# Optimization experiments

Measured on AMD Instinct MI355X. Metric: run time of the kernel, lower is better.

The kernel has to match this reference:

```python
import jax, jax.numpy as jnp
import numpy as np

B, S, I, H, HI = 1024, 64, 2048, 2048, 2048  # batch, num_high_states, input_dim, hidden_dim, high_dim
L = 4          # num recurrent layers
NH = 16        # num heads
HD = H // NH   # head dim
MAX_STEPS = 100


def setup_inputs() -> dict:
    key = jax.random.key(0)
    ks = iter(jax.random.split(key, 40))
    std = 0.02
    d = {}
    d["x"] = jax.random.normal(next(ks), (B, I), jnp.float32)
    d["high_state"] = jax.random.normal(next(ks), (B, HI), jnp.float32)
    d["high_states_history"] = jax.random.normal(next(ks), (B, S, HI), jnp.float32)
    d["hidden"] = jax.random.normal(next(ks), (L, B, H), jnp.float32) * 0.1
    # input projection + timestep embedding
    d["W_in"] = jax.random.normal(next(ks), (I, H), jnp.float32) * std
    d["b_in"] = jnp.zeros((H,), jnp.float32)
    d["ts_emb"] = jax.random.normal(next(ks), (MAX_STEPS, H), jnp.float32) * std
    # hierarchical attention projections
    d["Wq"] = jax.random.normal(next(ks), (H, H), jnp.float32) * std
    d["bq"] = jnp.zeros((H,), jnp.float32)
    d["Wk"] = jax.random.normal(next(ks), (HI, H), jnp.float32) * std
    d["bk"] = jnp.zeros((H,), jnp.float32)
    d["Wv"] = jax.random.normal(next(ks), (HI, H), jnp.float32) * std
    d["bv"] = jnp.zeros((H,), jnp.float32)
    d["Wo"] = jax.random.normal(next(ks), (H, H), jnp.float32) * std
    d["bo"] = jnp.zeros((H,), jnp.float32)
    # per-layer GRU-like gates, stacked over layers; Linear in = I+H = 2H
    for nm in ("Wu", "Wr", "Ws", "Wc"):
        d[nm] = jax.random.normal(next(ks), (L, 2 * H, H), jnp.float32) * std
    for nm in ("bu", "br", "bs", "bc"):
        d[nm] = jnp.zeros((L, H), jnp.float32)
    # layer norm
    d["ln_g"] = jnp.ones((H,), jnp.float32)
    d["ln_b"] = jnp.zeros((H,), jnp.float32)
    d["timestep"] = 5
    return d


def _forward(x, high_states_history, hidden, W_in, b_in, ts_emb,
             Wq, bq, Wk, bk, Wv, bv, Wo, bo,
             Wu, bu, Wr, br, Ws, bs, Wc, bc, ln_g, ln_b, timestep):
    # input projection + timestep encoding
    x = x @ W_in + b_in + ts_emb[timestep]  # [B,H]
    # hierarchical attention (single query per batch element)
    q = (x @ Wq + bq).reshape(B, NH, HD)
    k = (high_states_history @ Wk + bk).reshape(B, S, NH, HD)
    v = (high_states_history @ Wv + bv).reshape(B, S, NH, HD)
    scores = jnp.einsum("bhd,bshd->bhs", q, k) / np.sqrt(HD).astype(np.float32)
    attn = jax.nn.softmax(scores, axis=-1)  # [B,NH,S]
    ctx = jnp.einsum("bhs,bshd->bhd", attn, v).reshape(B, H)
    x = x + (ctx @ Wo + bo)
    # stacked GRU-like recurrent layers (loop over fixed small L)
    new_hidden = []
    for i in range(L):
        h = hidden[i]
        comb = jnp.concatenate([x, h], axis=1)  # [B,2H]
        u = jax.nn.sigmoid(comb @ Wu[i] + bu[i])
        r = jax.nn.sigmoid(comb @ Wr[i] + br[i])
        s = jax.nn.sigmoid(comb @ Ws[i] + bs[i])
        comb_r = jnp.concatenate([x, r * h], axis=1)
        cand = jax.nn.gelu(comb_r @ Wc[i] + bc[i], approximate=False)
        new_h = (1 - u) * h + u * (s * cand + (1 - s) * h)
        new_hidden.append(new_h)
        x = new_h  # dropout is identity in eval
    # layer norm (eps matches torch default 1e-5)
    mu = jnp.mean(x, axis=-1, keepdims=True)
    var = jnp.mean(jnp.square(x - mu), axis=-1, keepdims=True)
    out = (x - mu) * jax.lax.rsqrt(var + 1e-5) * ln_g + ln_b
    return out, jnp.stack(new_hidden)


def reference(x, high_state, high_states_history, hidden, W_in, b_in, ts_emb,
              Wq, bq, Wk, bk, Wv, bv, Wo, bo,
              Wu, bu, Wr, br, Ws, bs, Wc, bc, ln_g, ln_b, timestep):
    # high_state is accepted by the original signature but unused in the body
    return _forward(x, high_states_history, hidden, W_in, b_in, ts_emb,
                    Wq, bq, Wk, bk, Wv, bv, Wo, bo,
                    Wu, bu, Wr, br, Ws, bs, Wc, bc, ln_g, ln_b, timestep)
```

## Files before the change

kernel.cpp:

```cpp
#include <hip/hip_runtime.h>
#include <hip/hip_bf16.h>
#include <math.h>

#define B_  1024
#define S_  64
#define H_  2048
#define L_  4
#define NH_ 16
#define HD_ 128
#define WSLAB_ ((size_t)2048 * 4096)

typedef __attribute__((ext_vector_type(4))) float floatx4;
typedef __attribute__((ext_vector_type(8))) short shortx8;

__device__ __forceinline__ unsigned short f2bf(float f) {
  union { float f; unsigned int u; } v; v.f = f;
  unsigned int u = v.u;
  return (unsigned short)((u + 0x7fffu + ((u >> 16) & 1u)) >> 16);
}

__device__ __forceinline__ void gload16(const void* g, void* l) {
  __builtin_amdgcn_global_load_lds(
      (const __attribute__((address_space(1))) void*)g,
      (__attribute__((address_space(3))) void*)l, 16, 0, 0);
}

__global__ __launch_bounds__(256) void cvt_bf(
    const float* __restrict__ in, unsigned short* __restrict__ out, int n8)
{
  int i = blockIdx.x * 256 + threadIdx.x;
  if (i >= n8) return;
  const float4* p = (const float4*)in;
  float4 a = p[i * 2], b = p[i * 2 + 1];
  unsigned short o[8] = { f2bf(a.x), f2bf(a.y), f2bf(a.z), f2bf(a.w),
                          f2bf(b.x), f2bf(b.y), f2bf(b.z), f2bf(b.w) };
  ((uint4*)out)[i] = *(uint4*)o;
}

__global__ __launch_bounds__(256) void tconv4(
    const float* __restrict__ s0, const float* __restrict__ s1,
    const float* __restrict__ s2, const float* __restrict__ s3,
    unsigned short* __restrict__ dst, int K)
{
  const float* src = (blockIdx.z == 0) ? s0 : (blockIdx.z == 1) ? s1
                   : (blockIdx.z == 2) ? s2 : s3;
  unsigned short* out = dst + (size_t)blockIdx.z * 2048 * K;
  __shared__ float tile[64][65];
  int k0 = blockIdx.x * 64, n0 = blockIdx.y * 64;
  int t = threadIdx.x;
  int tr = t >> 4, tc = (t & 15) * 4;
  #pragma unroll
  for (int rep = 0; rep < 4; ++rep) {
    int kk = tr + rep * 16;
    float4 v = *(const float4*)(src + (size_t)(k0 + kk) * 2048 + n0 + tc);
    tile[kk][tc] = v.x; tile[kk][tc + 1] = v.y;
    tile[kk][tc + 2] = v.z; tile[kk][tc + 3] = v.w;
  }
  __syncthreads();
  int nr = t >> 2, kc = (t & 3) * 16;
  unsigned short o[16];
  #pragma unroll
  for (int j = 0; j < 16; ++j) o[j] = f2bf(tile[kc + j][nr]);
  *(uint4*)(out + (size_t)(n0 + nr) * K + k0 + kc)     = *(uint4*)&o[0];
  *(uint4*)(out + (size_t)(n0 + nr) * K + k0 + kc + 8) = *(uint4*)&o[8];
}

enum { EPI_XIN = 0, EPI_QB = 1, EPI_X2 = 2, EPI_GRU = 3, EPI_CTX = 4 };

template<int EPI>
__global__ __launch_bounds__(512) void gemm_w(
    int K, int bpitch, int koff,
    const unsigned short* __restrict__ A0,
    const unsigned short* __restrict__ BT,
    const float* __restrict__ b0,
    const float* __restrict__ tse, const int* __restrict__ tsp,
    const float* __restrict__ res,
    const float* __restrict__ Cc, const float* __restrict__ U,
    const float* __restrict__ Sg, const float* __restrict__ Hf,
    float* __restrict__ Cf, unsigned short* __restrict__ Cb)
{
  const int t = threadIdx.x, wid = t >> 6, lane = t & 63, lr = lane & 15, lg = lane >> 4;
  const int wr = wid >> 2, wc = wid & 3;
  const int g = blockIdx.x;
  const int m_base = (g >> 4) * 64;
  const int pn = g & 15;
  __shared__ unsigned short lds_a[64 * 32];
  __shared__ unsigned short lds_b[128 * 32];
  floatx4 acc[2][2] = {};
  const int arow = t >> 2, akc = t & 3;
  const int akcs = akc ^ ((arow >> 1) & 3);
  const int brow = t >> 2, bkc = t & 3;
  const int bkcs = bkc ^ ((brow >> 1) & 3);
  const int nkt = K >> 5;
  for (int kt = 0; kt < nkt; ++kt) {
    if (t < 256) {
      int gk = kt * 32 + akcs * 8;
      const unsigned short* ga;
      if (EPI == EPI_CTX) ga = A0 + ((size_t)(m_base + arow) * 16 + pn) * 2048 + gk;
      else                ga = A0 + (size_t)(m_base + arow) * K + gk;
      gload16(ga, &lds_a[wid * 512]);
    }
    {
      int gk = kt * 32 + bkcs * 8;
      const unsigned short* gb;
      if (EPI == EPI_CTX) gb = BT + (size_t)(pn * 128 + brow) * 2048 + gk;
      else                gb = BT + (size_t)((pn & 15) * 128 + brow) * bpitch + koff + gk;
      gload16(gb, &lds_b[wid * 512]);
    }
    __syncthreads();
    const int sl = lg ^ ((lr >> 1) & 3);
    shortx8 af[2], bfv[2];
    #pragma unroll
    for (int mt = 0; mt < 2; ++mt)
      af[mt] = *(shortx8*)&lds_a[(wr * 32 + mt * 16 + lr) * 32 + sl * 8];
    #pragma unroll
    for (int nt = 0; nt < 2; ++nt)
      bfv[nt] = *(shortx8*)&lds_b[(wc * 32 + nt * 16 + lr) * 32 + sl * 8];
    #pragma unroll
    for (int mt = 0; mt < 2; ++mt)
      #pragma unroll
      for (int nt = 0; nt < 2; ++nt)
        acc[mt][nt] = __builtin_amdgcn_mfma_f32_16x16x32_bf16(af[mt], bfv[nt], acc[mt][nt], 0, 0, 0);
    __syncthreads();
  }
  int ts = 0;
  if (EPI == EPI_XIN) ts = tsp[0];
  #pragma unroll
  for (int mt = 0; mt < 2; ++mt)
  #pragma unroll
  for (int nt = 0; nt < 2; ++nt)
  #pragma unroll
  for (int j = 0; j < 4; ++j) {
    int row = m_base + wr * 32 + mt * 16 + lg * 4 + j;
    int col = pn * 128 + wc * 32 + nt * 16 + lr;
    size_t idx = (size_t)row * 2048 + col;
    float v = acc[mt][nt][j] + b0[col];
    if (EPI == EPI_XIN) {
      v += tse[(size_t)ts * 2048 + col];
      Cf[idx] = v; Cb[idx] = f2bf(v);
    } else if (EPI == EPI_QB) {
      Cb[idx] = f2bf(v);
    } else if (EPI == EPI_X2) {
      v += res[idx]; Cb[idx] = f2bf(v);
    } else if (EPI == EPI_CTX) {
      Cb[idx] = f2bf(v);
    } else {
      v += Cc[idx];
      float gl = 0.5f * v * (1.f + erff(v * 0.70710678118654752f));
      float u = U[idx], s = Sg[idx], hh = Hf[idx];
      float nh = (1.f - u) * hh + u * (s * gl + (1.f - s) * hh);
      Cf[idx] = nh; Cb[idx] = f2bf(nh);
    }
  }
}

__global__ __launch_bounds__(256, 4) void gates_tconv(
    const unsigned short* __restrict__ Ax, const unsigned short* __restrict__ Ah,
    const unsigned short* __restrict__ TW,
    const float* __restrict__ bu, const float* __restrict__ br, const float* __restrict__ bs,
    const float* __restrict__ Hf,
    float* __restrict__ U, float* __restrict__ Sg,
    unsigned short* __restrict__ rh, float* __restrict__ Cc,
    const float* __restrict__ Wun, const float* __restrict__ Wrn,
    const float* __restrict__ Wsn, const float* __restrict__ Wcn,
    unsigned short* __restrict__ TWnext)
{
  __shared__ __align__(16) float smem[4224];
  const int t = threadIdx.x;
  if (blockIdx.x < 1024) {
    unsigned short* lds_a = (unsigned short*)smem;
    unsigned short* lds_b = (unsigned short*)smem + 2048;
    const int wid = t >> 6, lane = t & 63, lr = lane & 15, lg = lane >> 4;
    const int wr = wid >> 1, wc = wid & 1;
    const int g = blockIdx.x;
    const int m_base = (g >> 6) * 64;
    const int pan = g & 63;
    const int n_base = (pan & 15) * 128;
    const int z = pan >> 4;
    const unsigned short* BTz = TW + (size_t)z * WSLAB_;
    floatx4 acc[2][4] = {};
    const int nkt = (z == 3) ? 64 : 128;
    const int arow = t >> 2, akc = t & 3;
    const int akcs = akc ^ ((arow >> 1) & 3);
    for (int kt = 0; kt < nkt; ++kt) {
      {
        int gk = kt * 32 + akcs * 8;
        const unsigned short* ga;
        if (z == 3 || gk < 2048) ga = Ax + (size_t)(m_base + arow) * 2048 + gk;
        else                     ga = Ah + (size_t)(m_base + arow) * 2048 + (gk - 2048);
        gload16(ga, &lds_a[wid * 512]);
      }
      #pragma unroll
      for (int is = 0; is < 2; ++is) {
        int idx = is * 256 + t;
        int row = idx >> 2, kc = idx & 3;
        int kcs = kc ^ ((row >> 1) & 3);
        int gk = kt * 32 + kcs * 8;
        gload16(BTz + (size_t)(n_base + row) * 4096 + gk, &lds_b[(is * 256 + wid * 64) * 8]);
      }
      __syncthreads();
      const int sl = lg ^ ((lr >> 1) & 3);
      shortx8 af[2], bfv[4];
      #pragma unroll
      for (int mt = 0; mt < 2; ++mt)
        af[mt] = *(shortx8*)&lds_a[(wr * 32 + mt * 16 + lr) * 32 + sl * 8];
      #pragma unroll
      for (int nt = 0; nt < 4; ++nt)
        bfv[nt] = *(shortx8*)&lds_b[(wc * 64 + nt * 16 + lr) * 32 + sl * 8];
      #pragma unroll
      for (int mt = 0; mt < 2; ++mt)
        #pragma unroll
        for (int nt = 0; nt < 4; ++nt)
          acc[mt][nt] = __builtin_amdgcn_mfma_f32_16x16x32_bf16(af[mt], bfv[nt], acc[mt][nt], 0, 0, 0);
      __syncthreads();
    }
    #pragma unroll
    for (int mt = 0; mt < 2; ++mt)
    #pragma unroll
    for (int nt = 0; nt < 4; ++nt)
    #pragma unroll
    for (int j = 0; j < 4; ++j) {
      int row = m_base + wr * 32 + mt * 16 + lg * 4 + j;
      int col = n_base + wc * 64 + nt * 16 + lr;
      size_t idx = (size_t)row * 2048 + col;
      float v = acc[mt][nt][j];
      if (z == 0)      U[idx]  = 1.f / (1.f + expf(-(v + bu[col])));
      else if (z == 1) rh[idx] = f2bf((1.f / (1.f + expf(-(v + br[col])))) * Hf[idx]);
      else if (z == 2) Sg[idx] = 1.f / (1.f + expf(-(v + bs[col])));
      else             Cc[idx] = v;
    }
  } else {
    if (TWnext == nullptr) return;
    float (*tile)[65] = (float(*)[65])smem;
    int bid = blockIdx.x - 1024;
    int z = bid >> 11;
    int rem = bid & 2047;
    int k0 = (rem >> 5) * 64;
    int n0 = (rem & 31) * 64;
    const float* src = (z == 0) ? Wun : (z == 1) ? Wrn : (z == 2) ? Wsn : Wcn;
    unsigned short* outp = TWnext + (size_t)z * WSLAB_;
    int tr = t >> 4, tc = (t & 15) * 4;
    #pragma unroll
    for (int rep = 0; rep < 4; ++rep) {
      int kk = tr + rep * 16;
      float4 v = *(const float4*)(src + (size_t)(k0 + kk) * 2048 + n0 + tc);
      tile[kk][tc] = v.x; tile[kk][tc + 1] = v.y;
      tile[kk][tc + 2] = v.z; tile[kk][tc + 3] = v.w;
    }
    __syncthreads();
    int nr = t >> 2, kc = (t & 3) * 16;
    unsigned short o[16];
    #pragma unroll
    for (int j = 0; j < 16; ++j) o[j] = f2bf(tile[kc + j][nr]);
    *(uint4*)(outp + (size_t)(n0 + nr) * 4096 + k0 + kc)     = *(uint4*)&o[0];
    *(uint4*)(outp + (size_t)(n0 + nr) * 4096 + k0 + kc + 8) = *(uint4*)&o[8];
  }
}

__global__ __launch_bounds__(256) void gemm_t(
    const unsigned short* __restrict__ Q, const unsigned short* __restrict__ Wk,
    unsigned short* __restrict__ T)
{
  const int t = threadIdx.x, wid = t >> 6, lane = t & 63, lr = lane & 15, lg = lane >> 4;
  const int wr = wid >> 1, wc = wid & 1;
  const int h = blockIdx.z, m_base = blockIdx.x * 64, n_base = blockIdx.y * 128;
  __shared__ unsigned short lds_a[64 * 32], lds_b[128 * 32];
  floatx4 acc[2][4] = {};
  const int arow = t >> 2, akc = t & 3;
  const int akcs = akc ^ ((arow >> 1) & 3);
  for (int kt = 0; kt < 4; ++kt) {
    gload16(Q + (size_t)(m_base + arow) * 2048 + h * 128 + kt * 32 + akcs * 8,
            &lds_a[wid * 512]);
    #pragma unroll
    for (int is = 0; is < 2; ++is) {
      int idx = is * 256 + t;
      int row = idx >> 2, kc = idx & 3;
      int kcs = kc ^ ((row >> 1) & 3);
      gload16(Wk + (size_t)(n_base + row) * 2048 + h * 128 + kt * 32 + kcs * 8,
              &lds_b[(is * 256 + wid * 64) * 8]);
    }
    __syncthreads();
    const int sl = lg ^ ((lr >> 1) & 3);
    shortx8 af[2], bfv[4];
    #pragma unroll
    for (int mt = 0; mt < 2; ++mt)
      af[mt] = *(shortx8*)&lds_a[(wr * 32 + mt * 16 + lr) * 32 + sl * 8];
    #pragma unroll
    for (int nt = 0; nt < 4; ++nt)
      bfv[nt] = *(shortx8*)&lds_b[(wc * 64 + nt * 16 + lr) * 32 + sl * 8];
    #pragma unroll
    for (int mt = 0; mt < 2; ++mt)
      #pragma unroll
      for (int nt = 0; nt < 4; ++nt)
        acc[mt][nt] = __builtin_amdgcn_mfma_f32_16x16x32_bf16(af[mt], bfv[nt], acc[mt][nt], 0, 0, 0);
    __syncthreads();
  }
  #pragma unroll
  for (int mt = 0; mt < 2; ++mt)
  #pragma unroll
  for (int nt = 0; nt < 4; ++nt)
  #pragma unroll
  for (int j = 0; j < 4; ++j) {
    int row_o = m_base + wr * 32 + mt * 16 + lg * 4 + j;
    int col   = n_base + wc * 64 + nt * 16 + lr;
    T[((size_t)row_o * 16 + h) * 2048 + col] = f2bf(acc[mt][nt][j]);
  }
}

__global__ __launch_bounds__(256) void attn_fused(
    const unsigned short* __restrict__ T, const float* __restrict__ hist,
    unsigned short* __restrict__ Wb)
{
  const int t = threadIdx.x;
  const int wid = t >> 6, lane = t & 63, lr = lane & 15, lg = lane >> 4;
  const int b = blockIdx.x;
  __shared__ unsigned short lds_t[16 * 72];
  __shared__ unsigned short lds_h[64 * 72];
  __shared__ float sc[16 * 68];
  __shared__ float ps[64 * 16];
  floatx4 acc = {};
  for (int kt = 0; kt < 32; ++kt) {
    { int row = t >> 4, c4 = t & 15;
      int k = kt * 64 + c4 * 4;
      ushort4 v = *(const ushort4*)(T + ((size_t)b * 16 + row) * 2048 + k);
      *(ushort4*)&lds_t[row * 72 + c4 * 4] = v; }
    #pragma unroll
    for (int rep = 0; rep < 4; ++rep) {
      int idx = t + rep * 256;
      int srow = idx >> 4, c4 = idx & 15;
      int k = kt * 64 + c4 * 4;
      float4 hv = *(const float4*)(hist + ((size_t)b * 64 + srow) * 2048 + k);
      ushort4 uv; uv.x = f2bf(hv.x); uv.y = f2bf(hv.y); uv.z = f2bf(hv.z); uv.w = f2bf(hv.w);
      *(ushort4*)&lds_h[srow * 72 + c4 * 4] = uv;
    }
    __syncthreads();
    #pragma unroll
    for (int ks = 0; ks < 2; ++ks) {
      shortx8 af = *(shortx8*)&lds_t[lr * 72 + ks * 32 + lg * 8];
      shortx8 bv = *(shortx8*)&lds_h[(wid * 16 + lr) * 72 + ks * 32 + lg * 8];
      acc = __builtin_amdgcn_mfma_f32_16x16x32_bf16(af, bv, acc, 0, 0, 0);
    }
    __syncthreads();
  }
  #pragma unroll
  for (int j = 0; j < 4; ++j)
    sc[(lg * 4 + j) * 68 + wid * 16 + lr] = acc[j] * 0.088388347648318447f;
  __syncthreads();
  if (t < 64) {
    int h = t >> 2, qd = t & 3;
    float vv[16];
    float m = -1e30f;
    #pragma unroll
    for (int zz = 0; zz < 16; ++zz) { vv[zz] = sc[h * 68 + qd * 16 + zz]; m = fmaxf(m, vv[zz]); }
    m = fmaxf(m, __shfl_xor(m, 1)); m = fmaxf(m, __shfl_xor(m, 2));
    float sum = 0.f;
    #pragma unroll
    for (int zz = 0; zz < 16; ++zz) { vv[zz] = expf(vv[zz] - m); sum += vv[zz]; }
    sum += __shfl_xor(sum, 1); sum += __shfl_xor(sum, 2);
    float inv = 1.f / sum;
    #pragma unroll
    for (int zz = 0; zz < 16; ++zz)
      ps[(qd * 16 + zz) * 16 + h] = vv[zz] * inv;
  }
  __syncthreads();
  const int i0 = t * 8;
  floatx4 wacc[16][2] = {};
  const floatx4* ps4 = (const floatx4*)ps;
  for (int s = 0; s < 64; ++s) {
    const float* hp = hist + ((size_t)b * 64 + s) * 2048 + i0;
    float4 h4a = *(const float4*)hp;
    float4 h4b = *(const float4*)(hp + 4);
    floatx4 hva = { h4a.x, h4a.y, h4a.z, h4a.w };
    floatx4 hvb = { h4b.x, h4b.y, h4b.z, h4b.w };
    #pragma unroll
    for (int hq = 0; hq < 4; ++hq) {
      floatx4 p = ps4[s * 4 + hq];
      wacc[hq * 4 + 0][0] += p.x * hva; wacc[hq * 4 + 0][1] += p.x * hvb;
      wacc[hq * 4 + 1][0] += p.y * hva; wacc[hq * 4 + 1][1] += p.y * hvb;
      wacc[hq * 4 + 2][0] += p.z * hva; wacc[hq * 4 + 2][1] += p.z * hvb;
      wacc[hq * 4 + 3][0] += p.w * hva; wacc[hq * 4 + 3][1] += p.w * hvb;
    }
  }
  #pragma unroll
  for (int h = 0; h < 16; ++h) {
    unsigned short o[8];
    #pragma unroll
    for (int j = 0; j < 4; ++j) { o[j] = f2bf(wacc[h][0][j]); o[4 + j] = f2bf(wacc[h][1][j]); }
    *(uint4*)(Wb + ((size_t)b * 16 + h) * 2048 + i0) = *(uint4*)o;
  }
}

__global__ __launch_bounds__(256) void lnorm(
    const float* __restrict__ X, const float* __restrict__ gma,
    const float* __restrict__ bta, float* __restrict__ out)
{
  const int row = blockIdx.x, t = threadIdx.x;
  float4 a = *(const float4*)(X + (size_t)row * 2048 + t * 4);
  float4 c = *(const float4*)(X + (size_t)row * 2048 + 1024 + t * 4);
  float sum = a.x + a.y + a.z + a.w + c.x + c.y + c.z + c.w;
  float sq = a.x*a.x + a.y*a.y + a.z*a.z + a.w*a.w + c.x*c.x + c.y*c.y + c.z*c.z + c.w*c.w;
  #pragma unroll
  for (int off = 1; off < 64; off <<= 1) {
    sum += __shfl_xor(sum, off);
    sq  += __shfl_xor(sq, off);
  }
  __shared__ float red[8];
  int wid = t >> 6, lane = t & 63;
  if (lane == 0) { red[wid] = sum; red[wid + 4] = sq; }
  __syncthreads();
  sum = red[0] + red[1] + red[2] + red[3];
  sq  = red[4] + red[5] + red[6] + red[7];
  float mu = sum * (1.f / 2048.f);
  float var = sq * (1.f / 2048.f) - mu * mu;
  float rs = rsqrtf(var + 1e-5f);
  const float* pa = &a.x; const float* pc = &c.x;
  #pragma unroll
  for (int j = 0; j < 4; ++j) {
    int col = t * 4 + j;
    out[(size_t)row * 2048 + col] = (pa[j] - mu) * rs * gma[col] + bta[col];
  }
  #pragma unroll
  for (int j = 0; j < 4; ++j) {
    int col = 1024 + t * 4 + j;
    out[(size_t)row * 2048 + col] = (pc[j] - mu) * rs * gma[col] + bta[col];
  }
}

extern "C" void kernel_launch(void* const* d_in, const int* in_sizes, int n_in,
                              void* d_out, int out_size, void* d_ws, size_t ws_size,
                              hipStream_t stream) {
  (void)in_sizes; (void)n_in; (void)out_size; (void)ws_size;
  const float* x      = (const float*)d_in[0];
  const float* hist   = (const float*)d_in[2];
  const float* hidden = (const float*)d_in[3];
  const float* W_in   = (const float*)d_in[4];
  const float* b_in   = (const float*)d_in[5];
  const float* ts_emb = (const float*)d_in[6];
  const float* Wq     = (const float*)d_in[7];
  const float* bq     = (const float*)d_in[8];
  const float* Wk     = (const float*)d_in[9];
  const float* Wv     = (const float*)d_in[11];
  const float* bv     = (const float*)d_in[12];
  const float* Wo     = (const float*)d_in[13];
  const float* bo     = (const float*)d_in[14];
  const float* Wu     = (const float*)d_in[15];
  const float* Wr     = (const float*)d_in[16];
  const float* Wsg    = (const float*)d_in[17];
  const float* Wc     = (const float*)d_in[18];
  const float* bu     = (const float*)d_in[19];
  const float* br     = (const float*)d_in[20];
  const float* bs     = (const float*)d_in[21];
  const float* bc     = (const float*)d_in[22];
  const float* ln_g   = (const float*)d_in[23];
  const float* ln_b   = (const float*)d_in[24];
  const int*   tsp    = (const int*)d_in[25];
  float* out = (float*)d_out;

  const size_t BH = (size_t)B_ * H_;
  char* w = (char*)d_ws;
  auto take = [&](size_t bytes) { char* p = w; w += bytes; return p; };

  unsigned short* TW0  = (unsigned short*)take((size_t)4 * WSLAB_ * 2);
  unsigned short* TW1  = (unsigned short*)take((size_t)4 * WSLAB_ * 2);
  unsigned short* Tb   = (unsigned short*)take((size_t)B_ * 16 * 2048 * 2);
  unsigned short* WT4  = (unsigned short*)take((size_t)4 * H_ * H_ * 2);
  unsigned short* WinT = WT4;
  unsigned short* WqT  = WT4 + (size_t)H_ * H_;
  unsigned short* WvT  = WT4 + (size_t)2 * H_ * H_;
  unsigned short* WoT  = WT4 + (size_t)3 * H_ * H_;
  unsigned short* Wkb  = (unsigned short*)take((size_t)H_ * H_ * 2);
  unsigned short* x_bf   = (unsigned short*)take(BH * 2);
  unsigned short* h_bf   = (unsigned short*)take((size_t)L_ * BH * 2);
  unsigned short* xin_bf = (unsigned short*)take(BH * 2);
  unsigned short* q_bf   = (unsigned short*)take(BH * 2);
  unsigned short* ctx_bf = (unsigned short*)take(BH * 2);
  unsigned short* x2_bf  = (unsigned short*)take(BH * 2);
  unsigned short* rh_bf  = (unsigned short*)take(BH * 2);
  unsigned short* xa     = (unsigned short*)take(BH * 2);
  unsigned short* xb     = (unsigned short*)take(BH * 2);
  float* U   = (float*)take(BH * 4);
  float* Sg  = (float*)take(BH * 4);
  float* Cc  = (float*)take(BH * 4);
  float* XIN = out;

  dim3 blk(256);
  dim3 blkw(512);

  cvt_bf<<<dim3(1024), blk, 0, stream>>>(x, x_bf, (int)(BH / 8));
  cvt_bf<<<dim3(4096), blk, 0, stream>>>(hidden, h_bf, (int)(L_ * BH / 8));
  cvt_bf<<<dim3(2048), blk, 0, stream>>>(Wk, Wkb, (int)((size_t)H_ * H_ / 8));
  tconv4<<<dim3(32, 32, 4), blk, 0, stream>>>(W_in, Wq, Wv, Wo, WT4, 2048);
  tconv4<<<dim3(64, 32, 4), blk, 0, stream>>>(Wu, Wr, Wsg, Wc, TW0, 4096);

  gemm_w<EPI_XIN><<<dim3(256), blkw, 0, stream>>>(
      2048, 2048, 0, x_bf, WinT, b_in, ts_emb, tsp, nullptr,
      nullptr, nullptr, nullptr, nullptr, XIN, xin_bf);
  gemm_w<EPI_QB><<<dim3(256), blkw, 0, stream>>>(
      2048, 2048, 0, xin_bf, WqT, bq, nullptr, nullptr, nullptr,
      nullptr, nullptr, nullptr, nullptr, nullptr, q_bf);
  gemm_t<<<dim3(16, 16, 16), blk, 0, stream>>>(q_bf, Wkb, Tb);
  attn_fused<<<dim3(1024), blk, 0, stream>>>(Tb, hist, Tb);
  gemm_w<EPI_CTX><<<dim3(256), blkw, 0, stream>>>(
      2048, 2048, 0, Tb, WvT, bv, nullptr, nullptr, nullptr,
      nullptr, nullptr, nullptr, nullptr, nullptr, ctx_bf);
  gemm_w<EPI_X2><<<dim3(256), blkw, 0, stream>>>(
      2048, 2048, 0, ctx_bf, WoT, bo, nullptr, nullptr, XIN,
      nullptr, nullptr, nullptr, nullptr, nullptr, x2_bf);

  unsigned short* xcur = x2_bf;
  for (int i = 0; i < L_; ++i) {
    const float* h_i = hidden + (size_t)i * BH;
    float* nh_f = out + BH + (size_t)i * BH;
    unsigned short* nh_b = (i & 1) ? xb : xa;
    unsigned short* TWcur = (i & 1) ? TW1 : TW0;
    unsigned short* TWnxt = (i < 3) ? ((i & 1) ? TW0 : TW1) : nullptr;
    int grid = (i < 3) ? 9216 : 1024;
    size_t off = (size_t)(i + 1) * WSLAB_;
    gates_tconv<<<dim3(grid), blk, 0, stream>>>(
        xcur, h_bf + (size_t)i * BH, TWcur,
        bu + (size_t)i * H_, br + (size_t)i * H_, bs + (size_t)i * H_,
        h_i, U, Sg, rh_bf, Cc,
        Wu + off, Wr + off, Wsg + off, Wc + off, TWnxt);
    gemm_w<EPI_GRU><<<dim3(256), blkw, 0, stream>>>(
        2048, 4096, 2048, rh_bf, TWcur + (size_t)3 * WSLAB_,
        bc + (size_t)i * H_, nullptr, nullptr, nullptr,
        Cc, U, Sg, h_i, nh_f, nh_b);
    xcur = nh_b;
  }

  lnorm<<<dim3(1024), blk, 0, stream>>>(out + BH + (size_t)3 * BH, ln_g, ln_b, out);
}
```

Before: 1.273 ms.

## Overlap next-layer weight conversion with candidate GEMM and shrink square-GEMM tiles

The next layer's weight transpose/convert blocks move out of the gates GEMM launch and into the candidate GEMM launch, so they now run alongside the small candidate GEMM rather than the large gates GEMM. The 2048x2048 GEMMs switch from 512-thread 64x128 tiles to 256-thread 32x128 tiles with twice as many blocks, which gives more blocks across the CUs. The trade-off is more weight-tile reloads per output element and a rebalanced mix of GEMM and conversion blocks in the fused launches.

```diff
diff --git a/kernel.cpp b/kernel.cpp
--- a/kernel.cpp
+++ b/kernel.cpp
@@ -65,57 +65,51 @@
   *(uint4*)(out + (size_t)(n0 + nr) * K + k0 + kc + 8) = *(uint4*)&o[8];
 }
 
-enum { EPI_XIN = 0, EPI_QB = 1, EPI_X2 = 2, EPI_GRU = 3, EPI_CTX = 4 };
+enum { EPI_XIN = 0, EPI_QB = 1, EPI_X2 = 2, EPI_CTX = 3 };
 
 template<int EPI>
-__global__ __launch_bounds__(512) void gemm_w(
-    int K, int bpitch, int koff,
+__global__ __launch_bounds__(256, 2) void gemm32(
     const unsigned short* __restrict__ A0,
     const unsigned short* __restrict__ BT,
     const float* __restrict__ b0,
     const float* __restrict__ tse, const int* __restrict__ tsp,
     const float* __restrict__ res,
-    const float* __restrict__ Cc, const float* __restrict__ U,
-    const float* __restrict__ Sg, const float* __restrict__ Hf,
     float* __restrict__ Cf, unsigned short* __restrict__ Cb)
 {
   const int t = threadIdx.x, wid = t >> 6, lane = t & 63, lr = lane & 15, lg = lane >> 4;
-  const int wr = wid >> 2, wc = wid & 3;
   const int g = blockIdx.x;
-  const int m_base = (g >> 4) * 64;
+  const int m_base = (g >> 4) * 32;
   const int pn = g & 15;
-  __shared__ unsigned short lds_a[64 * 32];
+  __shared__ unsigned short lds_a[32 * 32];
   __shared__ unsigned short lds_b[128 * 32];
   floatx4 acc[2][2] = {};
   const int arow = t >> 2, akc = t & 3;
   const int akcs = akc ^ ((arow >> 1) & 3);
-  const int brow = t >> 2, bkc = t & 3;
-  const int bkcs = bkc ^ ((brow >> 1) & 3);
-  const int nkt = K >> 5;
-  for (int kt = 0; kt < nkt; ++kt) {
-    if (t < 256) {
+  for (int kt = 0; kt < 64; ++kt) {
+    if (t < 128) {
       int gk = kt * 32 + akcs * 8;
       const unsigned short* ga;
       if (EPI == EPI_CTX) ga = A0 + ((size_t)(m_base + arow) * 16 + pn) * 2048 + gk;
-      else                ga = A0 + (size_t)(m_base + arow) * K + gk;
+      else                ga = A0 + (size_t)(m_base + arow) * 2048 + gk;
       gload16(ga, &lds_a[wid * 512]);
     }
-    {
-      int gk = kt * 32 + bkcs * 8;
-      const unsigned short* gb;
-      if (EPI == EPI_CTX) gb = BT + (size_t)(pn * 128 + brow) * 2048 + gk;
-      else                gb = BT + (size_t)((pn & 15) * 128 + brow) * bpitch + koff + gk;
-      gload16(gb, &lds_b[wid * 512]);
+    #pragma unroll
+    for (int is = 0; is < 2; ++is) {
+      int idx = is * 256 + t;
+      int row = idx >> 2, kc = idx & 3;
+      int kcs = kc ^ ((row >> 1) & 3);
+      int gk = kt * 32 + kcs * 8;
+      gload16(BT + (size_t)(pn * 128 + row) * 2048 + gk, &lds_b[(is * 256 + wid * 64) * 8]);
     }
     __syncthreads();
     const int sl = lg ^ ((lr >> 1) & 3);
     shortx8 af[2], bfv[2];
     #pragma unroll
     for (int mt = 0; mt < 2; ++mt)
-      af[mt] = *(shortx8*)&lds_a[(wr * 32 + mt * 16 + lr) * 32 + sl * 8];
+      af[mt] = *(shortx8*)&lds_a[(mt * 16 + lr) * 32 + sl * 8];
     #pragma unroll
     for (int nt = 0; nt < 2; ++nt)
-      bfv[nt] = *(shortx8*)&lds_b[(wc * 32 + nt * 16 + lr) * 32 + sl * 8];
+      bfv[nt] = *(shortx8*)&lds_b[(wid * 32 + nt * 16 + lr) * 32 + sl * 8];
     #pragma unroll
     for (int mt = 0; mt < 2; ++mt)
       #pragma unroll
@@ -131,8 +125,8 @@
   for (int nt = 0; nt < 2; ++nt)
   #pragma unroll
   for (int j = 0; j < 4; ++j) {
-    int row = m_base + wr * 32 + mt * 16 + lg * 4 + j;
-    int col = pn * 128 + wc * 32 + nt * 16 + lr;
+    int row = m_base + mt * 16 + lg * 4 + j;
+    int col = pn * 128 + wid * 32 + nt * 16 + lr;
     size_t idx = (size_t)row * 2048 + col;
     float v = acc[mt][nt][j] + b0[col];
     if (EPI == EPI_XIN) {
@@ -142,97 +136,152 @@
       Cb[idx] = f2bf(v);
     } else if (EPI == EPI_X2) {
       v += res[idx]; Cb[idx] = f2bf(v);
-    } else if (EPI == EPI_CTX) {
+    } else {
       Cb[idx] = f2bf(v);
-    } else {
-      v += Cc[idx];
-      float gl = 0.5f * v * (1.f + erff(v * 0.70710678118654752f));
-      float u = U[idx], s = Sg[idx], hh = Hf[idx];
-      float nh = (1.f - u) * hh + u * (s * gl + (1.f - s) * hh);
-      Cf[idx] = nh; Cb[idx] = f2bf(nh);
-    }
-  }
-}
-
-__global__ __launch_bounds__(256, 4) void gates_tconv(
+    }
+  }
+}
+
+__global__ __launch_bounds__(256, 4) void gemm_gates(
     const unsigned short* __restrict__ Ax, const unsigned short* __restrict__ Ah,
     const unsigned short* __restrict__ TW,
     const float* __restrict__ bu, const float* __restrict__ br, const float* __restrict__ bs,
     const float* __restrict__ Hf,
     float* __restrict__ U, float* __restrict__ Sg,
-    unsigned short* __restrict__ rh, float* __restrict__ Cc,
+    unsigned short* __restrict__ rh, float* __restrict__ Cc)
+{
+  const int t = threadIdx.x, wid = t >> 6, lane = t & 63, lr = lane & 15, lg = lane >> 4;
+  const int wr = wid >> 1, wc = wid & 1;
+  const int g = blockIdx.x;
+  const int m_base = (g >> 6) * 64;
+  const int pan = g & 63;
+  const int n_base = (pan & 15) * 128;
+  const int z = pan >> 4;
+  const unsigned short* BTz = TW + (size_t)z * WSLAB_;
+  __shared__ unsigned short lds_a[64 * 32];
+  __shared__ unsigned short lds_b[128 * 32];
+  floatx4 acc[2][4] = {};
+  const int nkt = (z == 3) ? 64 : 128;
+  const int arow = t >> 2, akc = t & 3;
+  const int akcs = akc ^ ((arow >> 1) & 3);
+  for (int kt = 0; kt < nkt; ++kt) {
+    {
+      int gk = kt * 32 + akcs * 8;
+      const unsigned short* ga;
+      if (z == 3 || gk < 2048) ga = Ax + (size_t)(m_base + arow) * 2048 + gk;
+      else                     ga = Ah + (size_t)(m_base + arow) * 2048 + (gk - 2048);
+      gload16(ga, &lds_a[wid * 512]);
+    }
+    #pragma unroll
+    for (int is = 0; is < 2; ++is) {
+      int idx = is * 256 + t;
+      int row = idx >> 2, kc = idx & 3;
+      int kcs = kc ^ ((row >> 1) & 3);
+      int gk = kt * 32 + kcs * 8;
+      gload16(BTz + (size_t)(n_base + row) * 4096 + gk, &lds_b[(is * 256 + wid * 64) * 8]);
+    }
+    __syncthreads();
+    const int sl = lg ^ ((lr >> 1) & 3);
+    shortx8 af[2], bfv[4];
+    #pragma unroll
+    for (int mt = 0; mt < 2; ++mt)
+      af[mt] = *(shortx8*)&lds_a[(wr * 32 + mt * 16 + lr) * 32 + sl * 8];
+    #pragma unroll
+    for (int nt = 0; nt < 4; ++nt)
+      bfv[nt] = *(shortx8*)&lds_b[(wc * 64 + nt * 16 + lr) * 32 + sl * 8];
+    #pragma unroll
+    for (int mt = 0; mt < 2; ++mt)
+      #pragma unroll
+      for (int nt = 0; nt < 4; ++nt)
+        acc[mt][nt] = __builtin_amdgcn_mfma_f32_16x16x32_bf16(af[mt], bfv[nt], acc[mt][nt], 0, 0, 0);
+    __syncthreads();
+  }
+  #pragma unroll
+  for (int mt = 0; mt < 2; ++mt)
+  #pragma unroll
+  for (int nt = 0; nt < 4; ++nt)
+  #pragma unroll
+  for (int j = 0; j < 4; ++j) {
+    int row = m_base + wr * 32 + mt * 16 + lg * 4 + j;
+    int col = n_base + wc * 64 + nt * 16 + lr;
+    size_t idx = (size_t)row * 2048 + col;
+    float v = acc[mt][nt][j];
+    if (z == 0)      U[idx]  = 1.f / (1.f + expf(-(v + bu[col])));
+    else if (z == 1) rh[idx] = f2bf((1.f / (1.f + expf(-(v + br[col])))) * Hf[idx]);
+    else if (z == 2) Sg[idx] = 1.f / (1.f + expf(-(v + bs[col])));
+    else             Cc[idx] = v;
+  }
+}
+
+__global__ __launch_bounds__(256) void cand_tconv(
+    const unsigned short* __restrict__ Arh, const unsigned short* __restrict__ TW,
+    const float* __restrict__ bc, const float* __restrict__ Cc,
+    const float* __restrict__ U, const float* __restrict__ Sg,
+    const float* __restrict__ Hf,
+    float* __restrict__ nh_f, unsigned short* __restrict__ nh_b,
     const float* __restrict__ Wun, const float* __restrict__ Wrn,
     const float* __restrict__ Wsn, const float* __restrict__ Wcn,
     unsigned short* __restrict__ TWnext)
 {
   __shared__ __align__(16) float smem[4224];
   const int t = threadIdx.x;
-  if (blockIdx.x < 1024) {
+  if (blockIdx.x < 512) {
     unsigned short* lds_a = (unsigned short*)smem;
-    unsigned short* lds_b = (unsigned short*)smem + 2048;
+    unsigned short* lds_b = (unsigned short*)smem + 1024;
     const int wid = t >> 6, lane = t & 63, lr = lane & 15, lg = lane >> 4;
-    const int wr = wid >> 1, wc = wid & 1;
     const int g = blockIdx.x;
-    const int m_base = (g >> 6) * 64;
-    const int pan = g & 63;
-    const int n_base = (pan & 15) * 128;
-    const int z = pan >> 4;
-    const unsigned short* BTz = TW + (size_t)z * WSLAB_;
-    floatx4 acc[2][4] = {};
-    const int nkt = (z == 3) ? 64 : 128;
+    const int m_base = (g >> 4) * 32;
+    const int pn = g & 15;
+    const unsigned short* BTz = TW + (size_t)3 * WSLAB_;
+    floatx4 acc[2][2] = {};
     const int arow = t >> 2, akc = t & 3;
     const int akcs = akc ^ ((arow >> 1) & 3);
-    for (int kt = 0; kt < nkt; ++kt) {
-      {
-        int gk = kt * 32 + akcs * 8;
-        const unsigned short* ga;
-        if (z == 3 || gk < 2048) ga = Ax + (size_t)(m_base + arow) * 2048 + gk;
-        else                     ga = Ah + (size_t)(m_base + arow) * 2048 + (gk - 2048);
-        gload16(ga, &lds_a[wid * 512]);
-      }
+    for (int kt = 0; kt < 64; ++kt) {
+      if (t < 128)
+        gload16(Arh + (size_t)(m_base + arow) * 2048 + kt * 32 + akcs * 8, &lds_a[wid * 512]);
       #pragma unroll
       for (int is = 0; is < 2; ++is) {
         int idx = is * 256 + t;
         int row = idx >> 2, kc = idx & 3;
         int kcs = kc ^ ((row >> 1) & 3);
         int gk = kt * 32 + kcs * 8;
-        gload16(BTz + (size_t)(n_base + row) * 4096 + gk, &lds_b[(is * 256 + wid * 64) * 8]);
+        gload16(BTz + (size_t)(pn * 128 + row) * 4096 + 2048 + gk, &lds_b[(is * 256 + wid * 64) * 8]);
       }
       __syncthreads();
       const int sl = lg ^ ((lr >> 1) & 3);
-      shortx8 af[2], bfv[4];
+      shortx8 af[2], bfv[2];
       #pragma unroll
       for (int mt = 0; mt < 2; ++mt)
-        af[mt] = *(shortx8*)&lds_a[(wr * 32 + mt * 16 + lr) * 32 + sl * 8];
-      #pragma unroll
-      for (int nt = 0; nt < 4; ++nt)
-        bfv[nt] = *(shortx8*)&lds_b[(wc * 64 + nt * 16 + lr) * 32 + sl * 8];
+        af[mt] = *(shortx8*)&lds_a[(mt * 16 + lr) * 32 + sl * 8];
+      #pragma unroll
+      for (int nt = 0; nt < 2; ++nt)
+        bfv[nt] = *(shortx8*)&lds_b[(wid * 32 + nt * 16 + lr) * 32 + sl * 8];
       #pragma unroll
       for (int mt = 0; mt < 2; ++mt)
         #pragma unroll
-        for (int nt = 0; nt < 4; ++nt)
+        for (int nt = 0; nt < 2; ++nt)
           acc[mt][nt] = __builtin_amdgcn_mfma_f32_16x16x32_bf16(af[mt], bfv[nt], acc[mt][nt], 0, 0, 0);
       __syncthreads();
     }
     #pragma unroll
     for (int mt = 0; mt < 2; ++mt)
     #pragma unroll
-    for (int nt = 0; nt < 4; ++nt)
+    for (int nt = 0; nt < 2; ++nt)
     #pragma unroll
     for (int j = 0; j < 4; ++j) {
-      int row = m_base + wr * 32 + mt * 16 + lg * 4 + j;
-      int col = n_base + wc * 64 + nt * 16 + lr;
+      int row = m_base + mt * 16 + lg * 4 + j;
+      int col = pn * 128 + wid * 32 + nt * 16 + lr;
       size_t idx = (size_t)row * 2048 + col;
-      float v = acc[mt][nt][j];
-      if (z == 0)      U[idx]  = 1.f / (1.f + expf(-(v + bu[col])));
-      else if (z == 1) rh[idx] = f2bf((1.f / (1.f + expf(-(v + br[col])))) * Hf[idx]);
-      else if (z == 2) Sg[idx] = 1.f / (1.f + expf(-(v + bs[col])));
-      else             Cc[idx] = v;
+      float v = acc[mt][nt][j] + Cc[idx] + bc[col];
+      float gl = 0.5f * v * (1.f + erff(v * 0.70710678118654752f));
+      float u = U[idx], s = Sg[idx], hh = Hf[idx];
+      float nh = (1.f - u) * hh + u * (s * gl + (1.f - s) * hh);
+      nh_f[idx] = nh; nh_b[idx] = f2bf(nh);
     }
   } else {
     if (TWnext == nullptr) return;
     float (*tile)[65] = (float(*)[65])smem;
-    int bid = blockIdx.x - 1024;
+    int bid = blockIdx.x - 512;
     int z = bid >> 11;
     int rem = bid & 2047;
     int k0 = (rem >> 5) * 64;
@@ -484,7 +533,6 @@
   float* XIN = out;
 
   dim3 blk(256);
-  dim3 blkw(512);
 
   cvt_bf<<<dim3(1024), blk, 0, stream>>>(x, x_bf, (int)(BH / 8));
   cvt_bf<<<dim3(4096), blk, 0, stream>>>(hidden, h_bf, (int)(L_ * BH / 8));
@@ -492,20 +540,16 @@
   tconv4<<<dim3(32, 32, 4), blk, 0, stream>>>(W_in, Wq, Wv, Wo, WT4, 2048);
   tconv4<<<dim3(64, 32, 4), blk, 0, stream>>>(Wu, Wr, Wsg, Wc, TW0, 4096);
 
-  gemm_w<EPI_XIN><<<dim3(256), blkw, 0, stream>>>(
-      2048, 2048, 0, x_bf, WinT, b_in, ts_emb, tsp, nullptr,
-      nullptr, nullptr, nullptr, nullptr, XIN, xin_bf);
-  gemm_w<EPI_QB><<<dim3(256), blkw, 0, stream>>>(
-      2048, 2048, 0, xin_bf, WqT, bq, nullptr, nullptr, nullptr,
-      nullptr, nullptr, nullptr, nullptr, nullptr, q_bf);
+  gemm32<EPI_XIN><<<dim3(512), blk, 0, stream>>>(
+      x_bf, WinT, b_in, ts_emb, tsp, nullptr, XIN, xin_bf);
+  gemm32<EPI_QB><<<dim3(512), blk, 0, stream>>>(
+      xin_bf, WqT, bq, nullptr, nullptr, nullptr, nullptr, q_bf);
   gemm_t<<<dim3(16, 16, 16), blk, 0, stream>>>(q_bf, Wkb, Tb);
   attn_fused<<<dim3(1024), blk, 0, stream>>>(Tb, hist, Tb);
-  gemm_w<EPI_CTX><<<dim3(256), blkw, 0, stream>>>(
-      2048, 2048, 0, Tb, WvT, bv, nullptr, nullptr, nullptr,
-      nullptr, nullptr, nullptr, nullptr, nullptr, ctx_bf);
-  gemm_w<EPI_X2><<<dim3(256), blkw, 0, stream>>>(
-      2048, 2048, 0, ctx_bf, WoT, bo, nullptr, nullptr, XIN,
-      nullptr, nullptr, nullptr, nullptr, nullptr, x2_bf);
+  gemm32<EPI_CTX><<<dim3(512), blk, 0, stream>>>(
+      Tb, WvT, bv, nullptr, nullptr, nullptr, nullptr, ctx_bf);
+  gemm32<EPI_X2><<<dim3(512), blk, 0, stream>>>(
+      ctx_bf, WoT, bo, nullptr, nullptr, XIN, nullptr, x2_bf);
 
   unsigned short* xcur = x2_bf;
   for (int i = 0; i < L_; ++i) {
@@ -514,17 +558,15 @@
     unsigned short* nh_b = (i & 1) ? xb : xa;
     unsigned short* TWcur = (i & 1) ? TW1 : TW0;
     unsigned short* TWnxt = (i < 3) ? ((i & 1) ? TW0 : TW1) : nullptr;
-    int grid = (i < 3) ? 9216 : 1024;
-    size_t off = (size_t)(i + 1) * WSLAB_;
-    gates_tconv<<<dim3(grid), blk, 0, stream>>>(
+    gemm_gates<<<dim3(1024), blk, 0, stream>>>(
         xcur, h_bf + (size_t)i * BH, TWcur,
         bu + (size_t)i * H_, br + (size_t)i * H_, bs + (size_t)i * H_,
-        h_i, U, Sg, rh_bf, Cc,
+        h_i, U, Sg, rh_bf, Cc);
+    int grid = (i < 3) ? 8704 : 512;
+    size_t off = (size_t)(i + 1) * WSLAB_;
+    cand_tconv<<<dim3(grid), blk, 0, stream>>>(
+        rh_bf, TWcur, bc + (size_t)i * H_, Cc, U, Sg, h_i, nh_f, nh_b,
         Wu + off, Wr + off, Wsg + off, Wc + off, TWnxt);
-    gemm_w<EPI_GRU><<<dim3(256), blkw, 0, stream>>>(
-        2048, 4096, 2048, rh_bf, TWcur + (size_t)3 * WSLAB_,
-        bc + (size_t)i * H_, nullptr, nullptr, nullptr,
-        Cc, U, Sg, h_i, nh_f, nh_b);
     xcur = nh_b;
   }
 
```

Result: faster. 1.194 ms (-6.2%).
